# Kernel optimization log

Measured on AMD Instinct MI355X. Metric: run time of the kernel, lower is better.

## Reference

```python
import jax, jax.numpy as jnp
import numpy as np

N_NODES = 100000
N_EDGES = 1000000
IN_CH = 312
HID = 256
OUT = 256


def _sage_conv(x, src, dst, W_l, b_l, W_r, num_nodes):
    # PyG SAGEConv (mean aggr): out = mean_{j in N(i)} x_j @ W_l + b_l + x_i @ W_r
    msg = x[src]                                             # [E, C] gather
    agg = jax.ops.segment_sum(msg, dst, num_segments=num_nodes)  # [N, C]
    deg = jax.ops.segment_sum(jnp.ones((src.shape[0],), dtype=x.dtype), dst,
                              num_segments=num_nodes)        # [N]
    mean = agg / jnp.maximum(deg, 1.0)[:, None]
    return mean @ W_l + b_l + x @ W_r


def setup_inputs() -> dict:
    key = jax.random.key(0)
    ks = jax.random.split(key, 8)
    x = jax.random.normal(ks[0], (N_NODES, IN_CH), dtype=jnp.float32)
    edge_index = jax.random.randint(ks[1], (2, N_EDGES), 0, N_NODES, dtype=jnp.int64)
    s1 = 1.0 / np.sqrt(IN_CH)
    s2 = 1.0 / np.sqrt(HID)
    W1_l = jax.random.normal(ks[2], (IN_CH, HID), dtype=jnp.float32) * s1
    b1 = jnp.zeros((HID,), dtype=jnp.float32)
    W1_r = jax.random.normal(ks[3], (IN_CH, HID), dtype=jnp.float32) * s1
    W2_l = jax.random.normal(ks[4], (HID, OUT), dtype=jnp.float32) * s2
    b2 = jnp.zeros((OUT,), dtype=jnp.float32)
    W2_r = jax.random.normal(ks[5], (HID, OUT), dtype=jnp.float32) * s2
    return {"x": x, "edge_index": edge_index, "W1_l": W1_l, "b1": b1,
            "W1_r": W1_r, "W2_l": W2_l, "b2": b2, "W2_r": W2_r}


def reference(x, edge_index, W1_l, b1, W1_r, W2_l, b2, W2_r):
    src, dst = edge_index[0], edge_index[1]
    n = x.shape[0]
    h = _sage_conv(x, src, dst, W1_l, b1, W1_r, n)
    h = jax.nn.relu(h)
    out = _sage_conv(h, src, dst, W2_l, b2, W2_r, n)
    return out
```

## Files before the change

### kernel.cpp

```cpp
#include <hip/hip_runtime.h>
#include <hip/hip_bf16.h>
#include <cstdint>
#include <cstddef>

#define IN_CH 312
#define HID 256

typedef __attribute__((ext_vector_type(8))) short bf16x8;
typedef __attribute__((ext_vector_type(4))) float f32x4;
typedef __attribute__((ext_vector_type(8))) unsigned short ushort8;

__device__ __forceinline__ unsigned short f2bf(float f) {
    union { float f; unsigned u; } v; v.f = f;
    const unsigned r = v.u + 0x7FFFu + ((v.u >> 16) & 1u);
    return (unsigned short)(r >> 16);
}
__device__ __forceinline__ float bf2f(unsigned short s) {
    union { unsigned u; float f; } v; v.u = (unsigned)s << 16;
    return v.f;
}
__device__ __forceinline__ void gload_lds16(const void* g, void* l) {
    __builtin_amdgcn_global_load_lds(
        (const __attribute__((address_space(1))) void*)g,
        (__attribute__((address_space(3))) void*)l, 16, 0, 0);
}

__global__ void detect_idx_kernel(const void* __restrict__ ei, int* __restrict__ flag) {
    if (blockIdx.x == 0 && threadIdx.x == 0) {
        const int* p = (const int*)ei;
        int ok = 1;
        for (int i = 0; i < 64; ++i) ok &= (p[2 * i + 1] == 0);
        *flag = ok;
    }
}
__device__ __forceinline__ long long load_idx(const void* ei, long long i, bool is64) {
    return is64 ? ((const long long*)ei)[i] : (long long)((const int*)ei)[i];
}

__global__ void hist_kernel(const void* __restrict__ ei, const int* __restrict__ flag,
                            int* __restrict__ cnt, int E) {
    const int i = blockIdx.x * blockDim.x + threadIdx.x;
    if (i >= E) return;
    const bool is64 = (*flag != 0);
    atomicAdd(&cnt[load_idx(ei, (long long)E + i, is64)], 1);
}

__global__ void offsets_kernel(const int* __restrict__ cnt, int* __restrict__ counter,
                               int* __restrict__ beg, int* __restrict__ cur, int n) {
    const int i = blockIdx.x * blockDim.x + threadIdx.x;
    if (i >= n) return;
    const int b = atomicAdd(counter, cnt[i]);
    beg[i] = b;
    cur[i] = b;
}

__global__ void fill_kernel(const void* __restrict__ ei, const int* __restrict__ flag,
                            int* __restrict__ cur, int* __restrict__ col, int E) {
    const int i = blockIdx.x * blockDim.x + threadIdx.x;
    if (i >= E) return;
    const bool is64 = (*flag != 0);
    const long long s = load_idx(ei, i, is64);
    const long long d = load_idx(ei, (long long)E + i, is64);
    col[atomicAdd(&cur[d], 1)] = (int)s;
}

__global__ void convert_w_kernel(const float* __restrict__ Wl, const float* __restrict__ Wr,
                                 unsigned short* __restrict__ wt, int K, int Kpad) {
    const int tid = blockIdx.x * blockDim.x + threadIdx.x;
    if (tid >= 512 * Kpad) return;
    const int c = tid / Kpad;
    const int k = tid % Kpad;
    float v = 0.f;
    if (k < K) v = (c < 256) ? Wl[(size_t)k * 256 + c] : Wr[(size_t)k * 256 + (c - 256)];
    wt[(size_t)c * Kpad + k] = f2bf(v);
}

template <int KPAD, bool AFP32, bool ZBF16>
__global__ __launch_bounds__(512) void mfma_gemm_kernel(
    const void* __restrict__ Avoid,
    const unsigned short* __restrict__ WT,
    const float* __restrict__ bias,
    unsigned short* __restrict__ Y,
    void* __restrict__ Z,
    int M)
{
    __shared__ __align__(16) char smem[49152];
    short* a_lds = (short*)smem;
    short* b_lds = (short*)(smem + 16384);

    const int tid  = (int)threadIdx.x;
    const int lane = tid & 63;
    const int wid  = tid >> 6;
    const int wr = wid >> 1, wc = wid & 1;
    const int r0 = blockIdx.x * 128;
    const int c0 = blockIdx.y * 256;

    f32x4 acc[2][8];
    #pragma unroll
    for (int i = 0; i < 2; ++i)
        #pragma unroll
        for (int j = 0; j < 8; ++j) acc[i][j] = (f32x4)0.f;

    const int ldrow  = lane >> 3;
    const int schunk = (lane & 7) ^ ldrow;

    for (int kb = 0; kb < KPAD; kb += 64) {
        __syncthreads();
        #pragma unroll
        for (int j = 0; j < 4; ++j) {
            const int ld = wid * 4 + j;
            const int trow = ld * 8 + ldrow;
            gload_lds16(WT + (size_t)(c0 + trow) * KPAD + kb + schunk * 8,
                        (char*)b_lds + ld * 1024);
        }
        if (AFP32) {
            const float* A = (const float*)Avoid;
            float4 v[4];
            #pragma unroll
            for (int it = 0; it < 4; ++it) {
                const int idx = tid + it * 512;
                const int row = idx >> 4, q = idx & 15;
                const int gr = min(r0 + row, M - 1);
                const int gk = kb + q * 4;
                v[it] = (gk < IN_CH) ? *(const float4*)(A + (size_t)gr * IN_CH + gk)
                                     : make_float4(0.f, 0.f, 0.f, 0.f);
            }
            #pragma unroll
            for (int it = 0; it < 4; ++it) {
                const int idx = tid + it * 512;
                const int row = idx >> 4, q = idx & 15;
                ushort4 b4;
                b4.x = f2bf(v[it].x); b4.y = f2bf(v[it].y);
                b4.z = f2bf(v[it].z); b4.w = f2bf(v[it].w);
                const int byte = row * 128 + (((q >> 1) ^ (row & 7)) * 16) + (q & 1) * 8;
                *(ushort4*)((char*)a_lds + byte) = b4;
            }
        } else {
            const unsigned short* A = (const unsigned short*)Avoid;
            #pragma unroll
            for (int j = 0; j < 2; ++j) {
                const int ld = wid * 2 + j;
                const int trow = ld * 8 + ldrow;
                const int gr = min(r0 + trow, M - 1);
                gload_lds16(A + (size_t)gr * KPAD + kb + schunk * 8,
                            (char*)a_lds + ld * 1024);
            }
        }
        __syncthreads();

        #pragma unroll
        for (int ks = 0; ks < 2; ++ks) {
            bf16x8 af[2], bg[8];
            #pragma unroll
            for (int f = 0; f < 2; ++f) {
                const int arow = wr * 32 + f * 16 + (lane & 15);
                const int ach  = (ks * 4 + (lane >> 4)) ^ (arow & 7);
                af[f] = *(const bf16x8*)((const char*)a_lds + arow * 128 + ach * 16);
            }
            #pragma unroll
            for (int f = 0; f < 8; ++f) {
                const int brow = wc * 128 + f * 16 + (lane & 15);
                const int bch  = (ks * 4 + (lane >> 4)) ^ (brow & 7);
                bg[f] = *(const bf16x8*)((const char*)b_lds + brow * 128 + bch * 16);
            }
            #pragma unroll
            for (int fm = 0; fm < 2; ++fm)
                #pragma unroll
                for (int fn = 0; fn < 8; ++fn)
                    acc[fm][fn] = __builtin_amdgcn_mfma_f32_16x16x32_bf16(
                        af[fm], bg[fn], acc[fm][fn], 0, 0, 0);
        }
    }

    const bool isY = (c0 == 0);
    const int cloc = wc * 128 + (lane & 15);

    if (isY || ZBF16) {
        constexpr int CST = 264;
        short* c_lds = (short*)smem;
        float bv4[8];
        #pragma unroll
        for (int fn = 0; fn < 8; ++fn)
            bv4[fn] = isY ? 0.f : bias[cloc + fn * 16];
        #pragma unroll
        for (int h = 0; h < 2; ++h) {
            __syncthreads();
            if ((wr >> 1) == h) {
                const int lr0 = (wr & 1) * 32 + (lane >> 4) * 4;
                #pragma unroll
                for (int fm = 0; fm < 2; ++fm)
                    #pragma unroll
                    for (int fn = 0; fn < 8; ++fn)
                        #pragma unroll
                        for (int r = 0; r < 4; ++r)
                            c_lds[(lr0 + fm * 16 + r) * CST + cloc + fn * 16] =
                                (short)f2bf(acc[fm][fn][r] + bv4[fn]);
            }
            __syncthreads();
            const int row = tid >> 3;
            const int cb  = (tid & 7) * 32;
            const int gr  = r0 + h * 64 + row;
            if (gr < M) {
                unsigned short* dst = isY
                    ? (Y + (size_t)gr * 256 + cb)
                    : ((unsigned short*)Z + (size_t)gr * 256 + cb);
                #pragma unroll
                for (int j = 0; j < 4; ++j)
                    *(ushort8*)(dst + j * 8) =
                        *(const ushort8*)&c_lds[row * CST + cb + j * 8];
            }
        }
    } else {
        const int rbase = r0 + wr * 32 + (lane >> 4) * 4;
        #pragma unroll
        for (int fn = 0; fn < 8; ++fn) {
            const int gc = cloc + fn * 16;
            const float bvv = bias[gc];
            #pragma unroll
            for (int fm = 0; fm < 2; ++fm)
                #pragma unroll
                for (int r = 0; r < 4; ++r) {
                    const int gr = rbase + fm * 16 + r;
                    if (gr < M) ((float*)Z)[(size_t)gr * 256 + gc] = acc[fm][fn][r] + bvv;
                }
        }
    }
}

template <bool LAYER1>
__global__ void gather_agg_kernel(const unsigned short* __restrict__ Y,
                                  const int* __restrict__ beg_arr,
                                  const int* __restrict__ cnt,
                                  const int* __restrict__ col,
                                  const void* __restrict__ Z,
                                  void* __restrict__ OUT, int N)
{
    const long long gw = ((long long)blockIdx.x * blockDim.x + threadIdx.x) >> 6;
    if (gw >= N) return;
    const int w = (int)gw;
    const int lane = threadIdx.x & 63;
    const int c4 = lane * 4;
    const int beg = beg_arr[w];
    const int deg = cnt[w];
    const int end = beg + deg;

    float4 a0 = make_float4(0.f, 0.f, 0.f, 0.f);
    float4 a1 = make_float4(0.f, 0.f, 0.f, 0.f);
    int e = beg;
    for (; e + 3 < end; e += 4) {
        const int s0 = col[e], s1 = col[e + 1], s2 = col[e + 2], s3 = col[e + 3];
        const ushort4 v0 = *(const ushort4*)(Y + (size_t)s0 * 256 + c4);
        const ushort4 v1 = *(const ushort4*)(Y + (size_t)s1 * 256 + c4);
        const ushort4 v2 = *(const ushort4*)(Y + (size_t)s2 * 256 + c4);
        const ushort4 v3 = *(const ushort4*)(Y + (size_t)s3 * 256 + c4);
        a0.x += bf2f(v0.x) + bf2f(v1.x);  a1.x += bf2f(v2.x) + bf2f(v3.x);
        a0.y += bf2f(v0.y) + bf2f(v1.y);  a1.y += bf2f(v2.y) + bf2f(v3.y);
        a0.z += bf2f(v0.z) + bf2f(v1.z);  a1.z += bf2f(v2.z) + bf2f(v3.z);
        a0.w += bf2f(v0.w) + bf2f(v1.w);  a1.w += bf2f(v2.w) + bf2f(v3.w);
    }
    for (; e < end; ++e) {
        const ushort4 v0 = *(const ushort4*)(Y + (size_t)col[e] * 256 + c4);
        a0.x += bf2f(v0.x); a0.y += bf2f(v0.y);
        a0.z += bf2f(v0.z); a0.w += bf2f(v0.w);
    }
    float4 acc;
    acc.x = a0.x + a1.x; acc.y = a0.y + a1.y;
    acc.z = a0.z + a1.z; acc.w = a0.w + a1.w;

    const float inv = 1.0f / fmaxf((float)deg, 1.0f);
    float4 z;
    if (LAYER1) {
        const ushort4 zb = *(const ushort4*)((const unsigned short*)Z + (size_t)w * 256 + c4);
        z = make_float4(bf2f(zb.x), bf2f(zb.y), bf2f(zb.z), bf2f(zb.w));
    } else {
        z = *(const float4*)((const float*)Z + (size_t)w * 256 + c4);
    }
    float4 o;
    o.x = acc.x * inv + z.x;
    o.y = acc.y * inv + z.y;
    o.z = acc.z * inv + z.z;
    o.w = acc.w * inv + z.w;
    if (LAYER1) {
        o.x = fmaxf(o.x, 0.f); o.y = fmaxf(o.y, 0.f);
        o.z = fmaxf(o.z, 0.f); o.w = fmaxf(o.w, 0.f);
        ushort4 ob;
        ob.x = f2bf(o.x); ob.y = f2bf(o.y); ob.z = f2bf(o.z); ob.w = f2bf(o.w);
        *(ushort4*)((unsigned short*)OUT + (size_t)w * 256 + c4) = ob;
    } else {
        *(float4*)((float*)OUT + (size_t)w * 256 + c4) = o;
    }
}

extern "C" void kernel_launch(void* const* d_in, const int* in_sizes, int n_in,
                              void* d_out, int out_size, void* d_ws, size_t ws_size,
                              hipStream_t stream) {
    const float* x   = (const float*)d_in[0];
    const void*  ei  = d_in[1];
    const float* W1l = (const float*)d_in[2];
    const float* b1  = (const float*)d_in[3];
    const float* W1r = (const float*)d_in[4];
    const float* W2l = (const float*)d_in[5];
    const float* b2  = (const float*)d_in[6];
    const float* W2r = (const float*)d_in[7];

    const int N = in_sizes[0] / IN_CH;
    const int E = in_sizes[1] / 2;

    char* ws = (char*)d_ws;
    size_t off = 0;
    auto alloc = [&](size_t bytes) {
        void* p = ws + off;
        off = (off + bytes + 255) & ~(size_t)255;
        return p;
    };
    int* flag    = (int*)alloc(4);
    int* cnt     = (int*)alloc((size_t)(N + 1) * 4);
    int* counter = cnt + N;
    int* beg     = (int*)alloc((size_t)N * 4);
    int* cur     = (int*)alloc((size_t)N * 4);
    int* col     = (int*)alloc((size_t)E * 4);
    unsigned short* wt1 = (unsigned short*)alloc((size_t)512 * 320 * 2);
    unsigned short* wt2 = (unsigned short*)alloc((size_t)512 * 256 * 2);
    unsigned short* hb  = (unsigned short*)alloc((size_t)N * 256 * 2);
    unsigned short* y   = (unsigned short*)alloc((size_t)N * 256 * 2);

    float* out = (float*)d_out;
    unsigned short* z1 = (unsigned short*)d_out;

    hipMemsetAsync(cnt, 0, (size_t)(N + 1) * 4, stream);
    detect_idx_kernel<<<1, 64, 0, stream>>>(ei, flag);
    hist_kernel<<<(E + 255) / 256, 256, 0, stream>>>(ei, flag, cnt, E);
    offsets_kernel<<<(N + 255) / 256, 256, 0, stream>>>(cnt, counter, beg, cur, N);
    fill_kernel<<<(E + 255) / 256, 256, 0, stream>>>(ei, flag, cur, col, E);

    convert_w_kernel<<<(512 * 320 + 255) / 256, 256, 0, stream>>>(W1l, W1r, wt1, IN_CH, 320);
    convert_w_kernel<<<(512 * 256 + 255) / 256, 256, 0, stream>>>(W2l, W2r, wt2, HID, 256);

    const dim3 ggrid((N + 127) / 128, 2);

    mfma_gemm_kernel<320, true, true><<<ggrid, 512, 0, stream>>>(x, wt1, b1, y, z1, N);
    gather_agg_kernel<true><<<(N + 3) / 4, 256, 0, stream>>>(y, beg, cnt, col, z1, hb, N);

    mfma_gemm_kernel<256, false, false><<<ggrid, 512, 0, stream>>>(hb, wt2, b2, y, out, N);
    gather_agg_kernel<false><<<(N + 3) / 4, 256, 0, stream>>>(y, beg, cnt, col, out, out, N);
}
```

Baseline: 486.7 us.

## Replace LDS-staged GEMM with register-direct loads from MFMA-prepacked weights

Weights are prepacked into MFMA fragment order, so each lane loads its B fragment straight from global memory with one 16-byte load. A rows are also loaded directly into registers and converted per lane, which removes LDS staging and the per-iteration barriers of the main loop. Shared memory shrinks to the epilogue buffer and the kernel declares 4 blocks per CU. The cost is redundant global and L2 traffic, since every wave fetches its own A and B fragments with no reuse through LDS, and the per-thread A loads are less coalesced.

```diff
diff --git a/kernel.cpp b/kernel.cpp
--- a/kernel.cpp
+++ b/kernel.cpp
@@ -18,11 +18,6 @@
 __device__ __forceinline__ float bf2f(unsigned short s) {
     union { unsigned u; float f; } v; v.u = (unsigned)s << 16;
     return v.f;
-}
-__device__ __forceinline__ void gload_lds16(const void* g, void* l) {
-    __builtin_amdgcn_global_load_lds(
-        (const __attribute__((address_space(1))) void*)g,
-        (__attribute__((address_space(3))) void*)l, 16, 0, 0);
 }
 
 __global__ void detect_idx_kernel(const void* __restrict__ ei, int* __restrict__ flag) {
@@ -64,29 +59,39 @@
     col[atomicAdd(&cur[d], 1)] = (int)s;
 }
 
-__global__ void convert_w_kernel(const float* __restrict__ Wl, const float* __restrict__ Wr,
-                                 unsigned short* __restrict__ wt, int K, int Kpad) {
+__global__ void pack_w_kernel(const float* __restrict__ Wl, const float* __restrict__ Wr,
+                              unsigned short* __restrict__ wtp, int K, int Kpad) {
     const int tid = blockIdx.x * blockDim.x + threadIdx.x;
-    if (tid >= 512 * Kpad) return;
-    const int c = tid / Kpad;
-    const int k = tid % Kpad;
-    float v = 0.f;
-    if (k < K) v = (c < 256) ? Wl[(size_t)k * 256 + c] : Wr[(size_t)k * 256 + (c - 256)];
-    wt[(size_t)c * Kpad + k] = f2bf(v);
+    const int total = (Kpad / 32) * 32 * 64;
+    if (tid >= total) return;
+    const int k32 = tid >> 11;
+    const int rem = tid & 2047;
+    const int c16 = rem >> 6;
+    const int l   = rem & 63;
+    const int col = c16 * 16 + (l & 15);
+    const int kbase = k32 * 32 + (l >> 4) * 8;
+    ushort8 o;
+    #pragma unroll
+    for (int j = 0; j < 8; ++j) {
+        const int k = kbase + j;
+        float v = 0.f;
+        if (k < K) v = (col < 256) ? Wl[(size_t)k * 256 + col]
+                                   : Wr[(size_t)k * 256 + (col - 256)];
+        o[j] = f2bf(v);
+    }
+    *(ushort8*)(wtp + (size_t)tid * 8) = o;
 }
 
 template <int KPAD, bool AFP32, bool ZBF16>
-__global__ __launch_bounds__(512) void mfma_gemm_kernel(
+__global__ __launch_bounds__(512, 4) void reg_gemm_kernel(
     const void* __restrict__ Avoid,
-    const unsigned short* __restrict__ WT,
+    const unsigned short* __restrict__ WTP,
     const float* __restrict__ bias,
     unsigned short* __restrict__ Y,
     void* __restrict__ Z,
     int M)
 {
-    __shared__ __align__(16) char smem[49152];
-    short* a_lds = (short*)smem;
-    short* b_lds = (short*)(smem + 16384);
+    __shared__ short c_lds[64 * 264];
 
     const int tid  = (int)threadIdx.x;
     const int lane = tid & 63;
@@ -95,80 +100,55 @@
     const int r0 = blockIdx.x * 128;
     const int c0 = blockIdx.y * 256;
 
+    const int lrow = lane & 15;
+    const int kgrp = lane >> 4;
+
+    const int gr0 = min(r0 + wr * 32 + lrow, M - 1);
+    const int gr1 = min(r0 + wr * 32 + 16 + lrow, M - 1);
+
     f32x4 acc[2][8];
     #pragma unroll
     for (int i = 0; i < 2; ++i)
         #pragma unroll
         for (int j = 0; j < 8; ++j) acc[i][j] = (f32x4)0.f;
 
-    const int ldrow  = lane >> 3;
-    const int schunk = (lane & 7) ^ ldrow;
-
-    for (int kb = 0; kb < KPAD; kb += 64) {
-        __syncthreads();
-        #pragma unroll
-        for (int j = 0; j < 4; ++j) {
-            const int ld = wid * 4 + j;
-            const int trow = ld * 8 + ldrow;
-            gload_lds16(WT + (size_t)(c0 + trow) * KPAD + kb + schunk * 8,
-                        (char*)b_lds + ld * 1024);
-        }
+    const int c16b = (c0 >> 4) + wc * 8;
+
+    for (int kb = 0; kb < KPAD; kb += 32) {
+        const int k32 = kb >> 5;
+        const int k0 = kb + kgrp * 8;
+
+        bf16x8 af[2];
         if (AFP32) {
             const float* A = (const float*)Avoid;
-            float4 v[4];
-            #pragma unroll
-            for (int it = 0; it < 4; ++it) {
-                const int idx = tid + it * 512;
-                const int row = idx >> 4, q = idx & 15;
-                const int gr = min(r0 + row, M - 1);
-                const int gk = kb + q * 4;
-                v[it] = (gk < IN_CH) ? *(const float4*)(A + (size_t)gr * IN_CH + gk)
-                                     : make_float4(0.f, 0.f, 0.f, 0.f);
-            }
-            #pragma unroll
-            for (int it = 0; it < 4; ++it) {
-                const int idx = tid + it * 512;
-                const int row = idx >> 4, q = idx & 15;
-                ushort4 b4;
-                b4.x = f2bf(v[it].x); b4.y = f2bf(v[it].y);
-                b4.z = f2bf(v[it].z); b4.w = f2bf(v[it].w);
-                const int byte = row * 128 + (((q >> 1) ^ (row & 7)) * 16) + (q & 1) * 8;
-                *(ushort4*)((char*)a_lds + byte) = b4;
+            if (k0 < IN_CH) {
+                const float4 a00 = *(const float4*)(A + (size_t)gr0 * IN_CH + k0);
+                const float4 a01 = *(const float4*)(A + (size_t)gr0 * IN_CH + k0 + 4);
+                const float4 a10 = *(const float4*)(A + (size_t)gr1 * IN_CH + k0);
+                const float4 a11 = *(const float4*)(A + (size_t)gr1 * IN_CH + k0 + 4);
+                af[0][0] = (short)f2bf(a00.x); af[0][1] = (short)f2bf(a00.y);
+                af[0][2] = (short)f2bf(a00.z); af[0][3] = (short)f2bf(a00.w);
+                af[0][4] = (short)f2bf(a01.x); af[0][5] = (short)f2bf(a01.y);
+                af[0][6] = (short)f2bf(a01.z); af[0][7] = (short)f2bf(a01.w);
+                af[1][0] = (short)f2bf(a10.x); af[1][1] = (short)f2bf(a10.y);
+                af[1][2] = (short)f2bf(a10.z); af[1][3] = (short)f2bf(a10.w);
+                af[1][4] = (short)f2bf(a11.x); af[1][5] = (short)f2bf(a11.y);
+                af[1][6] = (short)f2bf(a11.z); af[1][7] = (short)f2bf(a11.w);
+            } else {
+                af[0] = (bf16x8)0; af[1] = (bf16x8)0;
             }
         } else {
             const unsigned short* A = (const unsigned short*)Avoid;
-            #pragma unroll
-            for (int j = 0; j < 2; ++j) {
-                const int ld = wid * 2 + j;
-                const int trow = ld * 8 + ldrow;
-                const int gr = min(r0 + trow, M - 1);
-                gload_lds16(A + (size_t)gr * KPAD + kb + schunk * 8,
-                            (char*)a_lds + ld * 1024);
-            }
+            af[0] = *(const bf16x8*)(A + (size_t)gr0 * KPAD + k0);
+            af[1] = *(const bf16x8*)(A + (size_t)gr1 * KPAD + k0);
         }
-        __syncthreads();
-
-        #pragma unroll
-        for (int ks = 0; ks < 2; ++ks) {
-            bf16x8 af[2], bg[8];
-            #pragma unroll
-            for (int f = 0; f < 2; ++f) {
-                const int arow = wr * 32 + f * 16 + (lane & 15);
-                const int ach  = (ks * 4 + (lane >> 4)) ^ (arow & 7);
-                af[f] = *(const bf16x8*)((const char*)a_lds + arow * 128 + ach * 16);
-            }
-            #pragma unroll
-            for (int f = 0; f < 8; ++f) {
-                const int brow = wc * 128 + f * 16 + (lane & 15);
-                const int bch  = (ks * 4 + (lane >> 4)) ^ (brow & 7);
-                bg[f] = *(const bf16x8*)((const char*)b_lds + brow * 128 + bch * 16);
-            }
-            #pragma unroll
-            for (int fm = 0; fm < 2; ++fm)
-                #pragma unroll
-                for (int fn = 0; fn < 8; ++fn)
-                    acc[fm][fn] = __builtin_amdgcn_mfma_f32_16x16x32_bf16(
-                        af[fm], bg[fn], acc[fm][fn], 0, 0, 0);
+
+        const unsigned short* wp = WTP + (((size_t)(k32 * 32 + c16b)) << 9) + lane * 8;
+        #pragma unroll
+        for (int fn = 0; fn < 8; ++fn) {
+            const bf16x8 bg = *(const bf16x8*)(wp + ((size_t)fn << 9));
+            acc[0][fn] = __builtin_amdgcn_mfma_f32_16x16x32_bf16(af[0], bg, acc[0][fn], 0, 0, 0);
+            acc[1][fn] = __builtin_amdgcn_mfma_f32_16x16x32_bf16(af[1], bg, acc[1][fn], 0, 0, 0);
         }
     }
 
@@ -177,7 +157,6 @@
 
     if (isY || ZBF16) {
         constexpr int CST = 264;
-        short* c_lds = (short*)smem;
         float bv4[8];
         #pragma unroll
         for (int fn = 0; fn < 8; ++fn)
@@ -319,8 +298,8 @@
     int* beg     = (int*)alloc((size_t)N * 4);
     int* cur     = (int*)alloc((size_t)N * 4);
     int* col     = (int*)alloc((size_t)E * 4);
-    unsigned short* wt1 = (unsigned short*)alloc((size_t)512 * 320 * 2);
-    unsigned short* wt2 = (unsigned short*)alloc((size_t)512 * 256 * 2);
+    unsigned short* wtp1 = (unsigned short*)alloc((size_t)10 * 32 * 64 * 8 * 2);
+    unsigned short* wtp2 = (unsigned short*)alloc((size_t)8 * 32 * 64 * 8 * 2);
     unsigned short* hb  = (unsigned short*)alloc((size_t)N * 256 * 2);
     unsigned short* y   = (unsigned short*)alloc((size_t)N * 256 * 2);
 
@@ -333,14 +312,14 @@
     offsets_kernel<<<(N + 255) / 256, 256, 0, stream>>>(cnt, counter, beg, cur, N);
     fill_kernel<<<(E + 255) / 256, 256, 0, stream>>>(ei, flag, cur, col, E);
 
-    convert_w_kernel<<<(512 * 320 + 255) / 256, 256, 0, stream>>>(W1l, W1r, wt1, IN_CH, 320);
-    convert_w_kernel<<<(512 * 256 + 255) / 256, 256, 0, stream>>>(W2l, W2r, wt2, HID, 256);
+    pack_w_kernel<<<(10 * 32 * 64 + 255) / 256, 256, 0, stream>>>(W1l, W1r, wtp1, IN_CH, 320);
+    pack_w_kernel<<<(8 * 32 * 64 + 255) / 256, 256, 0, stream>>>(W2l, W2r, wtp2, HID, 256);
 
     const dim3 ggrid((N + 127) / 128, 2);
 
-    mfma_gemm_kernel<320, true, true><<<ggrid, 512, 0, stream>>>(x, wt1, b1, y, z1, N);
+    reg_gemm_kernel<320, true, true><<<ggrid, 512, 0, stream>>>(x, wtp1, b1, y, z1, N);
     gather_agg_kernel<true><<<(N + 3) / 4, 256, 0, stream>>>(y, beg, cnt, col, z1, hb, N);
 
-    mfma_gemm_kernel<256, false, false><<<ggrid, 512, 0, stream>>>(hb, wt2, b2, y, out, N);
+    reg_gemm_kernel<256, false, false><<<ggrid, 512, 0, stream>>>(hb, wtp2, b2, y, out, N);
     gather_agg_kernel<false><<<(N + 3) / 4, 256, 0, stream>>>(y, beg, cnt, col, out, out, N);
 }
```

New measurement: 570.3 us. 1.17x slower.

## Pre-pack weights in MFMA fragment order and load B directly from global

Applied to the files above, without the earlier changes.

Weights are now packed once into the per-lane MFMA fragment layout. The GEMM then reads B fragments straight from global/L2 with 16-byte vector loads, so B is no longer staged through LDS. This removes the B LDS traffic and LDS footprint, which leaves LDS sized only for A and the epilogue. In exchange, every wave re-reads B from global memory for each k-step, which relies on L2/L1 hits and adds global-load latency directly in front of the MFMAs.

```diff
diff --git a/kernel.cpp b/kernel.cpp
--- a/kernel.cpp
+++ b/kernel.cpp
@@ -64,29 +64,40 @@
     col[atomicAdd(&cur[d], 1)] = (int)s;
 }
 
-__global__ void convert_w_kernel(const float* __restrict__ Wl, const float* __restrict__ Wr,
-                                 unsigned short* __restrict__ wt, int K, int Kpad) {
+__global__ void pack_w_kernel(const float* __restrict__ Wl, const float* __restrict__ Wr,
+                              unsigned short* __restrict__ wtp, int K, int Kpad) {
     const int tid = blockIdx.x * blockDim.x + threadIdx.x;
-    if (tid >= 512 * Kpad) return;
-    const int c = tid / Kpad;
-    const int k = tid % Kpad;
-    float v = 0.f;
-    if (k < K) v = (c < 256) ? Wl[(size_t)k * 256 + c] : Wr[(size_t)k * 256 + (c - 256)];
-    wt[(size_t)c * Kpad + k] = f2bf(v);
+    const int total = (Kpad / 32) * 32 * 64;
+    if (tid >= total) return;
+    const int k32 = tid >> 11;
+    const int rem = tid & 2047;
+    const int c16 = rem >> 6;
+    const int l   = rem & 63;
+    const int col = c16 * 16 + (l & 15);
+    const int kbase = k32 * 32 + (l >> 4) * 8;
+    ushort8 o;
+    #pragma unroll
+    for (int j = 0; j < 8; ++j) {
+        const int k = kbase + j;
+        float v = 0.f;
+        if (k < K) v = (col < 256) ? Wl[(size_t)k * 256 + col]
+                                   : Wr[(size_t)k * 256 + (col - 256)];
+        o[j] = f2bf(v);
+    }
+    *(ushort8*)(wtp + (size_t)tid * 8) = o;
 }
 
 template <int KPAD, bool AFP32, bool ZBF16>
 __global__ __launch_bounds__(512) void mfma_gemm_kernel(
     const void* __restrict__ Avoid,
-    const unsigned short* __restrict__ WT,
+    const unsigned short* __restrict__ WTP,
     const float* __restrict__ bias,
     unsigned short* __restrict__ Y,
     void* __restrict__ Z,
     int M)
 {
-    __shared__ __align__(16) char smem[49152];
+    __shared__ __align__(16) char smem[64 * 264 * 2];
     short* a_lds = (short*)smem;
-    short* b_lds = (short*)(smem + 16384);
 
     const int tid  = (int)threadIdx.x;
     const int lane = tid & 63;
@@ -95,6 +106,9 @@
     const int r0 = blockIdx.x * 128;
     const int c0 = blockIdx.y * 256;
 
+    const int lrow = lane & 15;
+    const int kgrp = lane >> 4;
+
     f32x4 acc[2][8];
     #pragma unroll
     for (int i = 0; i < 2; ++i)
@@ -104,15 +118,10 @@
     const int ldrow  = lane >> 3;
     const int schunk = (lane & 7) ^ ldrow;
 
+    const int c16b = (c0 >> 4) + wc * 8;
+
     for (int kb = 0; kb < KPAD; kb += 64) {
         __syncthreads();
-        #pragma unroll
-        for (int j = 0; j < 4; ++j) {
-            const int ld = wid * 4 + j;
-            const int trow = ld * 8 + ldrow;
-            gload_lds16(WT + (size_t)(c0 + trow) * KPAD + kb + schunk * 8,
-                        (char*)b_lds + ld * 1024);
-        }
         if (AFP32) {
             const float* A = (const float*)Avoid;
             float4 v[4];
@@ -150,25 +159,21 @@
 
         #pragma unroll
         for (int ks = 0; ks < 2; ++ks) {
-            bf16x8 af[2], bg[8];
+            bf16x8 af[2];
             #pragma unroll
             for (int f = 0; f < 2; ++f) {
-                const int arow = wr * 32 + f * 16 + (lane & 15);
-                const int ach  = (ks * 4 + (lane >> 4)) ^ (arow & 7);
+                const int arow = wr * 32 + f * 16 + lrow;
+                const int ach  = (ks * 4 + kgrp) ^ (arow & 7);
                 af[f] = *(const bf16x8*)((const char*)a_lds + arow * 128 + ach * 16);
             }
-            #pragma unroll
-            for (int f = 0; f < 8; ++f) {
-                const int brow = wc * 128 + f * 16 + (lane & 15);
-                const int bch  = (ks * 4 + (lane >> 4)) ^ (brow & 7);
-                bg[f] = *(const bf16x8*)((const char*)b_lds + brow * 128 + bch * 16);
-            }
-            #pragma unroll
-            for (int fm = 0; fm < 2; ++fm)
-                #pragma unroll
-                for (int fn = 0; fn < 8; ++fn)
-                    acc[fm][fn] = __builtin_amdgcn_mfma_f32_16x16x32_bf16(
-                        af[fm], bg[fn], acc[fm][fn], 0, 0, 0);
+            const unsigned short* wp =
+                WTP + (((size_t)(((kb >> 5) + ks) * 32 + c16b)) << 9) + lane * 8;
+            #pragma unroll
+            for (int fn = 0; fn < 8; ++fn) {
+                const bf16x8 bg = *(const bf16x8*)(wp + ((size_t)fn << 9));
+                acc[0][fn] = __builtin_amdgcn_mfma_f32_16x16x32_bf16(af[0], bg, acc[0][fn], 0, 0, 0);
+                acc[1][fn] = __builtin_amdgcn_mfma_f32_16x16x32_bf16(af[1], bg, acc[1][fn], 0, 0, 0);
+            }
         }
     }
 
@@ -319,8 +324,8 @@
     int* beg     = (int*)alloc((size_t)N * 4);
     int* cur     = (int*)alloc((size_t)N * 4);
     int* col     = (int*)alloc((size_t)E * 4);
-    unsigned short* wt1 = (unsigned short*)alloc((size_t)512 * 320 * 2);
-    unsigned short* wt2 = (unsigned short*)alloc((size_t)512 * 256 * 2);
+    unsigned short* wtp1 = (unsigned short*)alloc((size_t)10 * 32 * 64 * 8 * 2);
+    unsigned short* wtp2 = (unsigned short*)alloc((size_t)8 * 32 * 64 * 8 * 2);
     unsigned short* hb  = (unsigned short*)alloc((size_t)N * 256 * 2);
     unsigned short* y   = (unsigned short*)alloc((size_t)N * 256 * 2);
 
@@ -333,14 +338,14 @@
     offsets_kernel<<<(N + 255) / 256, 256, 0, stream>>>(cnt, counter, beg, cur, N);
     fill_kernel<<<(E + 255) / 256, 256, 0, stream>>>(ei, flag, cur, col, E);
 
-    convert_w_kernel<<<(512 * 320 + 255) / 256, 256, 0, stream>>>(W1l, W1r, wt1, IN_CH, 320);
-    convert_w_kernel<<<(512 * 256 + 255) / 256, 256, 0, stream>>>(W2l, W2r, wt2, HID, 256);
+    pack_w_kernel<<<(10 * 32 * 64 + 255) / 256, 256, 0, stream>>>(W1l, W1r, wtp1, IN_CH, 320);
+    pack_w_kernel<<<(8 * 32 * 64 + 255) / 256, 256, 0, stream>>>(W2l, W2r, wtp2, HID, 256);
 
     const dim3 ggrid((N + 127) / 128, 2);
 
-    mfma_gemm_kernel<320, true, true><<<ggrid, 512, 0, stream>>>(x, wt1, b1, y, z1, N);
+    mfma_gemm_kernel<320, true, true><<<ggrid, 512, 0, stream>>>(x, wtp1, b1, y, z1, N);
     gather_agg_kernel<true><<<(N + 3) / 4, 256, 0, stream>>>(y, beg, cnt, col, z1, hb, N);
 
-    mfma_gemm_kernel<256, false, false><<<ggrid, 512, 0, stream>>>(hb, wt2, b2, y, out, N);
+    mfma_gemm_kernel<256, false, false><<<ggrid, 512, 0, stream>>>(hb, wtp2, b2, y, out, N);
     gather_agg_kernel<false><<<(N + 3) / 4, 256, 0, stream>>>(y, beg, cnt, col, out, out, N);
 }
```

Measured after the change: 555.3 us. 1.14x slower.

## Double-buffer GEMM K-loop with 32-wide stages to overlap loads and MFMA

Applied to the files above, without the earlier changes.

Restructures the MFMA GEMM main loop from single-buffered 64-wide K tiles into double-buffered 32-wide stages in the same shared memory. The next stage's global-to-LDS loads (and fp32 register loads for the A operand) are issued before the current stage's MFMAs, leaving one barrier per stage. The aim is to hide global memory latency behind compute. The cost is twice as many iterations and barriers, each doing half the work, and a different swizzle layout.

```diff
diff --git a/kernel.cpp b/kernel.cpp
--- a/kernel.cpp
+++ b/kernel.cpp
@@ -84,9 +84,8 @@
     void* __restrict__ Z,
     int M)
 {
+    constexpr int NS = KPAD / 32;
     __shared__ __align__(16) char smem[49152];
-    short* a_lds = (short*)smem;
-    short* b_lds = (short*)(smem + 16384);
 
     const int tid  = (int)threadIdx.x;
     const int lane = tid & 63;
@@ -95,81 +94,97 @@
     const int r0 = blockIdx.x * 128;
     const int c0 = blockIdx.y * 256;
 
+    const int lrow = lane & 15;
+    const int kgrp = lane >> 4;
+
     f32x4 acc[2][8];
     #pragma unroll
     for (int i = 0; i < 2; ++i)
         #pragma unroll
         for (int j = 0; j < 8; ++j) acc[i][j] = (f32x4)0.f;
 
-    const int ldrow  = lane >> 3;
-    const int schunk = (lane & 7) ^ ldrow;
-
-    for (int kb = 0; kb < KPAD; kb += 64) {
+    const int glrow = lane >> 2;
+    const int glc   = (lane & 3) ^ (glrow & 3);
+
+    const int srow = tid >> 2;
+    const int sc   = tid & 3;
+    const int sgr  = min(r0 + srow, M - 1);
+    const int swbyte = srow * 64 + ((sc ^ (srow & 3)) * 16);
+
+    auto stageB = [&](int t, int b) {
+        char* bb = smem + 16384 + b * 16384;
+        const int kb = t * 32;
+        #pragma unroll
+        for (int j = 0; j < 2; ++j) {
+            const int ld = wid * 2 + j;
+            const int row = ld * 16 + glrow;
+            gload_lds16(WT + (size_t)(c0 + row) * KPAD + kb + glc * 8,
+                        bb + ld * 1024);
+        }
+    };
+    auto stageA_g = [&](int t, int b) {
+        char* ab = smem + b * 8192;
+        const unsigned short* A = (const unsigned short*)Avoid;
+        const int row = wid * 16 + glrow;
+        const int gr = min(r0 + row, M - 1);
+        gload_lds16(A + (size_t)gr * KPAD + t * 32 + glc * 8, ab + wid * 1024);
+    };
+    float4 va, vb;
+    auto loadA_r = [&](int t) {
+        const float* A = (const float*)Avoid;
+        const int gk = t * 32 + sc * 8;
+        if (gk < IN_CH) {
+            va = *(const float4*)(A + (size_t)sgr * IN_CH + gk);
+            vb = *(const float4*)(A + (size_t)sgr * IN_CH + gk + 4);
+        } else {
+            va = make_float4(0.f, 0.f, 0.f, 0.f);
+            vb = make_float4(0.f, 0.f, 0.f, 0.f);
+        }
+    };
+    auto writeA = [&](int b) {
+        ushort8 o;
+        o[0] = f2bf(va.x); o[1] = f2bf(va.y); o[2] = f2bf(va.z); o[3] = f2bf(va.w);
+        o[4] = f2bf(vb.x); o[5] = f2bf(vb.y); o[6] = f2bf(vb.z); o[7] = f2bf(vb.w);
+        *(ushort8*)(smem + b * 8192 + swbyte) = o;
+    };
+    auto compute = [&](int b) {
+        const char* ab = smem + b * 8192;
+        const char* bb = smem + 16384 + b * 16384;
+        bf16x8 af[2], bg[8];
+        #pragma unroll
+        for (int f = 0; f < 2; ++f) {
+            const int arow = wr * 32 + f * 16 + lrow;
+            const int p = kgrp ^ (arow & 3);
+            af[f] = *(const bf16x8*)(ab + arow * 64 + p * 16);
+        }
+        #pragma unroll
+        for (int fn = 0; fn < 8; ++fn) {
+            const int brow = wc * 128 + fn * 16 + lrow;
+            const int p = kgrp ^ (brow & 3);
+            bg[fn] = *(const bf16x8*)(bb + brow * 64 + p * 16);
+        }
+        #pragma unroll
+        for (int fn = 0; fn < 8; ++fn) {
+            acc[0][fn] = __builtin_amdgcn_mfma_f32_16x16x32_bf16(af[0], bg[fn], acc[0][fn], 0, 0, 0);
+            acc[1][fn] = __builtin_amdgcn_mfma_f32_16x16x32_bf16(af[1], bg[fn], acc[1][fn], 0, 0, 0);
+        }
+    };
+
+    stageB(0, 0);
+    if (AFP32) { loadA_r(0); writeA(0); }
+    else       { stageA_g(0, 0); }
+    __syncthreads();
+
+    for (int t = 0; t < NS; ++t) {
+        const int b = t & 1, nb = b ^ 1;
+        if (t + 1 < NS) {
+            stageB(t + 1, nb);
+            if (AFP32) loadA_r(t + 1);
+            else       stageA_g(t + 1, nb);
+        }
+        compute(b);
+        if (AFP32 && t + 1 < NS) writeA(nb);
         __syncthreads();
-        #pragma unroll
-        for (int j = 0; j < 4; ++j) {
-            const int ld = wid * 4 + j;
-            const int trow = ld * 8 + ldrow;
-            gload_lds16(WT + (size_t)(c0 + trow) * KPAD + kb + schunk * 8,
-                        (char*)b_lds + ld * 1024);
-        }
-        if (AFP32) {
-            const float* A = (const float*)Avoid;
-            float4 v[4];
-            #pragma unroll
-            for (int it = 0; it < 4; ++it) {
-                const int idx = tid + it * 512;
-                const int row = idx >> 4, q = idx & 15;
-                const int gr = min(r0 + row, M - 1);
-                const int gk = kb + q * 4;
-                v[it] = (gk < IN_CH) ? *(const float4*)(A + (size_t)gr * IN_CH + gk)
-                                     : make_float4(0.f, 0.f, 0.f, 0.f);
-            }
-            #pragma unroll
-            for (int it = 0; it < 4; ++it) {
-                const int idx = tid + it * 512;
-                const int row = idx >> 4, q = idx & 15;
-                ushort4 b4;
-                b4.x = f2bf(v[it].x); b4.y = f2bf(v[it].y);
-                b4.z = f2bf(v[it].z); b4.w = f2bf(v[it].w);
-                const int byte = row * 128 + (((q >> 1) ^ (row & 7)) * 16) + (q & 1) * 8;
-                *(ushort4*)((char*)a_lds + byte) = b4;
-            }
-        } else {
-            const unsigned short* A = (const unsigned short*)Avoid;
-            #pragma unroll
-            for (int j = 0; j < 2; ++j) {
-                const int ld = wid * 2 + j;
-                const int trow = ld * 8 + ldrow;
-                const int gr = min(r0 + trow, M - 1);
-                gload_lds16(A + (size_t)gr * KPAD + kb + schunk * 8,
-                            (char*)a_lds + ld * 1024);
-            }
-        }
-        __syncthreads();
-
-        #pragma unroll
-        for (int ks = 0; ks < 2; ++ks) {
-            bf16x8 af[2], bg[8];
-            #pragma unroll
-            for (int f = 0; f < 2; ++f) {
-                const int arow = wr * 32 + f * 16 + (lane & 15);
-                const int ach  = (ks * 4 + (lane >> 4)) ^ (arow & 7);
-                af[f] = *(const bf16x8*)((const char*)a_lds + arow * 128 + ach * 16);
-            }
-            #pragma unroll
-            for (int f = 0; f < 8; ++f) {
-                const int brow = wc * 128 + f * 16 + (lane & 15);
-                const int bch  = (ks * 4 + (lane >> 4)) ^ (brow & 7);
-                bg[f] = *(const bf16x8*)((const char*)b_lds + brow * 128 + bch * 16);
-            }
-            #pragma unroll
-            for (int fm = 0; fm < 2; ++fm)
-                #pragma unroll
-                for (int fn = 0; fn < 8; ++fn)
-                    acc[fm][fn] = __builtin_amdgcn_mfma_f32_16x16x32_bf16(
-                        af[fm], bg[fn], acc[fm][fn], 0, 0, 0);
-        }
     }
 
     const bool isY = (c0 == 0);
```

Measured after the change: 480.2 us. About the same (-1.3%).
